# Kernel tuning notes

Hardware: AMD Instinct MI355X
Metric: run time of the kernel (lower is better)

## Reference

```python
import jax, jax.numpy as jnp
import numpy as np


def setup_inputs() -> dict:
    key = jax.random.key(0)
    ks = jax.random.split(key, 8)
    B, C, W, H = 4, 256, 64, 64
    Cq = C // 8
    return {
        "input": jax.random.normal(ks[0], (B, C, W, H), dtype=jnp.float32),
        "Wf": jax.random.normal(ks[1], (Cq, C), dtype=jnp.float32) * 0.05,
        "bf": jax.random.normal(ks[2], (Cq,), dtype=jnp.float32) * 0.05,
        "Wg": jax.random.normal(ks[3], (Cq, C), dtype=jnp.float32) * 0.05,
        "bg": jax.random.normal(ks[4], (Cq,), dtype=jnp.float32) * 0.05,
        "Wh": jax.random.normal(ks[5], (C, C), dtype=jnp.float32) * 0.05,
        "bh": jax.random.normal(ks[6], (C,), dtype=jnp.float32) * 0.05,
        "gamma": jax.random.normal(ks[7], (1,), dtype=jnp.float32),
    }


def reference(input, Wf, bf, Wg, bg, Wh, bh, gamma):
    # input: [B, C, W, H]; SAGAN self-attention over N = W*H spatial tokens.
    B, C, W, H = input.shape
    N = W * H
    x = input.reshape(B, C, N)
    # 1x1 Conv1d == per-token linear projection over channels.
    f = jnp.einsum('oc,bcn->bon', Wf, x) + bf[None, :, None]  # [B, C/8, N]
    g = jnp.einsum('oc,bcn->bon', Wg, x) + bg[None, :, None]  # [B, C/8, N]
    h = jnp.einsum('oc,bcn->bon', Wh, x) + bh[None, :, None]  # [B, C,   N]
    # s = f^T g -> [B, N, N]; softmax over last dim (columns / g-tokens).
    s = jnp.einsum('bon,bom->bnm', f, g)
    attention = jax.nn.softmax(s, axis=-1)
    # out = h @ attention^T : out[b,c,m] = sum_n h[b,c,n] * attention[b,m,n]
    out = jnp.einsum('bcn,bmn->bcm', h, attention)
    out = out.reshape(B, C, W, H)
    return gamma[0] * out + input
```

## Files before the change

### kernel.cpp

```cpp
#include <hip/hip_runtime.h>

typedef _Float16 half8 __attribute__((ext_vector_type(8)));
typedef _Float16 half4 __attribute__((ext_vector_type(4)));
typedef float floatx16 __attribute__((ext_vector_type(16)));

#define MFMA_F16(A, B, C) __builtin_amdgcn_mfma_f32_32x32x16_f16(A, B, C, 0, 0, 0)

constexpr int Bn = 4;
constexpr int Cc = 256;
constexpr int Cq = 32;
constexpr int Nn = 4096;
constexpr float LOG2E = 1.44269504088896340736f;


__device__ inline floatx16 zero16() {
  floatx16 z;
#pragma unroll
  for (int i = 0; i < 16; ++i) z[i] = 0.f;
  return z;
}

__global__ __launch_bounds__(256) void k_wconv(
    const float* __restrict__ Wf, const float* __restrict__ Wg,
    const float* __restrict__ Wh, _Float16* __restrict__ Wfh,
    _Float16* __restrict__ Wgh, _Float16* __restrict__ Whh) {
  int e = (blockIdx.x * 256 + threadIdx.x) * 4;
  const float* src;
  _Float16* dst;
  float sc = 1.f;
  if (e < 8192) { src = Wf + e; dst = Wfh + e; sc = LOG2E; }
  else if (e < 16384) { src = Wg + (e - 8192); dst = Wgh + (e - 8192); }
  else { src = Wh + (e - 16384); dst = Whh + (e - 16384); }
  float4 v = *(const float4*)src;
  half4 o;
  o[0] = (_Float16)(v.x * sc); o[1] = (_Float16)(v.y * sc);
  o[2] = (_Float16)(v.z * sc); o[3] = (_Float16)(v.w * sc);
  *(half4*)dst = o;
}

__global__ __launch_bounds__(256) void k_proj(
    const float* __restrict__ x,
    const _Float16* __restrict__ Wfh, const float* __restrict__ bf,
    const _Float16* __restrict__ Wgh, const float* __restrict__ bg,
    const _Float16* __restrict__ Whh, const float* __restrict__ bh,
    _Float16* __restrict__ Q, _Float16* __restrict__ K4,
    _Float16* __restrict__ V8) {
  int tid = threadIdx.x;
  int w = tid >> 6, lane = tid & 63;
  int ml = lane & 31, h = lane >> 5;
  int b = blockIdx.x >> 7, nt = blockIdx.x & 127;
  int n0 = nt * 32;
  const float* xb = x + (size_t)b * Cc * Nn + n0 + ml;

  for (int t = w; t < 10; t += 4) {
    const _Float16* W;
    const float* bias;
    float bscale = 1.f;
    int o0 = 0;
    if (t == 0) { W = Wfh; bias = bf; bscale = LOG2E; }
    else if (t == 1) { W = Wgh; bias = bg; }
    else { W = Whh + (size_t)(t - 2) * 32 * Cc; bias = bh + (t - 2) * 32; o0 = (t - 2) * 32; }

    floatx16 acc = zero16();
    const _Float16* wp = W + (size_t)ml * Cc + h * 8;
#pragma unroll
    for (int kc = 0; kc < 16; ++kc) {
      half8 a = *(const half8*)(wp + kc * 16);
      const float* xp = xb + (size_t)(kc * 16 + h * 8) * Nn;
      half8 bfr;
#pragma unroll
      for (int j = 0; j < 8; ++j) bfr[j] = (_Float16)xp[(size_t)j * Nn];
      acc = MFMA_F16(a, bfr, acc);
    }

    if (t == 0) {
      _Float16* op = Q + ((size_t)b * Nn + n0 + ml) * Cq;
#pragma unroll
      for (int qd = 0; qd < 4; ++qd) {
        float4 bq = *(const float4*)(bias + 8 * qd + 4 * h);
        const float* bqp = (const float*)&bq;
#pragma unroll
        for (int i = 0; i < 4; ++i) {
          int crow = i + 8 * qd + 4 * h;
          op[crow] = (_Float16)(acc[4 * qd + i] + bqp[i] * bscale);
        }
      }
    } else if (t == 1) {
#pragma unroll
      for (int qd = 0; qd < 4; ++qd) {
        float4 bq = *(const float4*)(bias + 8 * qd + 4 * h);
        const float* bqp = (const float*)&bq;
#pragma unroll
        for (int i = 0; i < 4; ++i) {
          int crow = i + 8 * qd + 4 * h;
          K4[(((size_t)b * 4 + (crow >> 3)) * Nn + n0 + ml) * 8 + (crow & 7)] =
              (_Float16)(acc[4 * qd + i] + bqp[i]);
        }
      }
    } else {
      size_t nb = (size_t)((n0 + ml) >> 3);
      _Float16* op = V8 + (((size_t)b * 512 + nb) * 256) * 8 + (ml & 7);
#pragma unroll
      for (int qd = 0; qd < 4; ++qd) {
        float4 bq = *(const float4*)(bias + 8 * qd + 4 * h);
        const float* bqp = (const float*)&bq;
#pragma unroll
        for (int i = 0; i < 4; ++i) {
          int crow = i + 8 * qd + 4 * h;
          op[(size_t)(o0 + crow) * 8] = (_Float16)(acc[4 * qd + i] + bqp[i]);
        }
      }
    }
  }
}

__global__ __launch_bounds__(512) void k_rowmax(const _Float16* __restrict__ Q,
                                                const _Float16* __restrict__ K4,
                                                float* __restrict__ M) {
  __shared__ float red[8][32];
  int tid = threadIdx.x, w = tid >> 6, lane = tid & 63;
  int ml = lane & 31, h = lane >> 5;
  int b = blockIdx.x >> 7, mt = blockIdx.x & 127;
  int m0 = mt * 32;
  const _Float16* qp = Q + ((size_t)b * Nn + m0 + ml) * Cq + h * 8;
  half8 qb0 = *(const half8*)(qp);
  half8 qb1 = *(const half8*)(qp + 16);
  const _Float16* kp0 = K4 + (((size_t)b * 4 + h) * Nn + w * 512 + ml) * 8;
  const _Float16* kp1 = K4 + (((size_t)b * 4 + 2 + h) * Nn + w * 512 + ml) * 8;
  float mx = -3.0e38f;
  for (int t = 0; t < 16; ++t) {
    floatx16 s = zero16();
    half8 k0 = *(const half8*)(kp0 + (size_t)t * 32 * 8);
    half8 k1 = *(const half8*)(kp1 + (size_t)t * 32 * 8);
    s = MFMA_F16(k0, qb0, s);
    s = MFMA_F16(k1, qb1, s);
#pragma unroll
    for (int i = 0; i < 16; ++i) mx = fmaxf(mx, s[i]);
  }
  mx = fmaxf(mx, __shfl_xor(mx, 32, 64));
  if (h == 0) red[w][ml] = mx;
  __syncthreads();
  if (tid < 32) {
    float m2 = red[0][tid];
#pragma unroll
    for (int i = 1; i < 8; ++i) m2 = fmaxf(m2, red[i][tid]);
    M[(size_t)b * Nn + m0 + tid] = m2;
  }
}

__global__ __launch_bounds__(512, 4) void k_attn(
    const _Float16* __restrict__ Q, const _Float16* __restrict__ K4,
    const _Float16* __restrict__ V8, const float* __restrict__ M,
    _Float16* __restrict__ Opart, float* __restrict__ lpart, int nspan) {
  __shared__ _Float16 P[2 * 64 * 128];
  __shared__ float lred[8][32];
  int tid = threadIdx.x, w = tid >> 6, lane = tid & 63;
  int ml = lane & 31, h = lane >> 5;
  int msub = w & 1, nq = w >> 1;
  int bx = blockIdx.x;
  int mt = bx & 63, b = (bx >> 6) & 3, nc = bx >> 8;
  int m0 = mt * 64;
  int nbase0 = nc * nspan;
  int sw = ml & 15;

  const _Float16* qp = Q + ((size_t)b * Nn + m0 + msub * 32 + ml) * Cq + h * 8;
  half8 qb0 = *(const half8*)(qp);
  half8 qb1 = *(const half8*)(qp + 16);
  float Mv = M[(size_t)b * Nn + m0 + msub * 32 + ml];
  float lacc = 0.f;

  const _Float16* k4b0 =
      K4 + (((size_t)b * 4 + h) * Nn + nbase0 + nq * 32 + ml) * 8;
  const _Float16* k4b1 =
      K4 + (((size_t)b * 4 + 2 + h) * Nn + nbase0 + nq * 32 + ml) * 8;

  int c0 = w * 32;
  const _Float16* v8b =
      V8 + (((size_t)b * 512 + (nbase0 >> 3)) * 256 + c0 + ml) * 8;

  floatx16 o0 = zero16(), o1 = zero16();
  int iters = nspan >> 7;
  _Float16* pwbase = &P[(msub * 32 + ml) * 128];
  const _Float16* pr0 = &P[ml * 128];
  const _Float16* pr1 = &P[(32 + ml) * 128];

  for (int it = 0; it < iters; ++it) {
    int bufo = (it & 1) * (64 * 128);
    {
      floatx16 s = zero16();
      half8 k0 = *(const half8*)(k4b0 + (size_t)it * 128 * 8);
      half8 k1 = *(const half8*)(k4b1 + (size_t)it * 128 * 8);
      s = MFMA_F16(k0, qb0, s);
      s = MFMA_F16(k1, qb1, s);
      _Float16* pw = pwbase + bufo;
#pragma unroll
      for (int q = 0; q < 4; ++q) {
        float p0 = exp2f(s[4 * q + 0] - Mv);
        float p1 = exp2f(s[4 * q + 1] - Mv);
        float p2 = exp2f(s[4 * q + 2] - Mv);
        float p3 = exp2f(s[4 * q + 3] - Mv);
        lacc += (p0 + p1) + (p2 + p3);
        half4 pk;
        pk[0] = (_Float16)p0; pk[1] = (_Float16)p1;
        pk[2] = (_Float16)p2; pk[3] = (_Float16)p3;
        *(half4*)(pw + ((nq * 4 + q) ^ sw) * 8 + 4 * h) = pk;
      }
    }
    __syncthreads();
    {
      const _Float16* vp = v8b + (size_t)it * 16 * 2048;
      const _Float16* p0b = pr0 + bufo;
      const _Float16* p1b = pr1 + bufo;
#pragma unroll
      for (int kc = 0; kc < 8; ++kc) {
        half8 vf = *(const half8*)(vp + (size_t)(kc * 2 + h) * 2048);
        int chunk = (kc * 2 + h) ^ sw;
        half8 pb0 = *(const half8*)(p0b + chunk * 8);
        half8 pb1 = *(const half8*)(p1b + chunk * 8);
        o0 = MFMA_F16(vf, pb0, o0);
        o1 = MFMA_F16(vf, pb1, o1);
      }
    }
  }

  lacc += __shfl_xor(lacc, 32, 64);
  if (h == 0) lred[w][ml] = lacc;
  __syncthreads();
  if (w < 2 && h == 0) {
    float lsum = lred[w][ml] + lred[w + 2][ml] + lred[w + 4][ml] + lred[w + 6][ml];
    lpart[((size_t)nc * Bn + b) * Nn + m0 + w * 32 + ml] = lsum;
  }

  _Float16* op0 = Opart + ((size_t)((size_t)nc * Bn + b) * Cc) * Nn + (m0 + ml);
#pragma unroll
  for (int r = 0; r < 16; ++r) {
    int c = c0 + (r & 3) + 8 * (r >> 2) + 4 * h;
    op0[(size_t)c * Nn] = (_Float16)o0[r];
    op0[(size_t)c * Nn + 32] = (_Float16)o1[r];
  }
}

__global__ __launch_bounds__(256) void k_fin(const _Float16* __restrict__ Op,
                                             const float* __restrict__ lp,
                                             const float* __restrict__ inp,
                                             const float* __restrict__ gamma,
                                             float* __restrict__ out, int NC) {
  int i4 = (blockIdx.x * 256 + threadIdx.x) * 4;
  int m = i4 & (Nn - 1);
  int bc = i4 >> 12;
  int b = bc >> 8;
  float ax = 0.f, ay = 0.f, az = 0.f, aw = 0.f;
  float lx = 0.f, ly = 0.f, lz = 0.f, lw = 0.f;
  for (int nc = 0; nc < NC; ++nc) {
    half4 o = *(const half4*)(Op + ((size_t)nc * Bn * Cc + bc) * Nn + m);
    float4 lv = *(const float4*)(lp + ((size_t)nc * Bn + b) * Nn + m);
    ax += (float)o[0]; ay += (float)o[1]; az += (float)o[2]; aw += (float)o[3];
    lx += lv.x; ly += lv.y; lz += lv.z; lw += lv.w;
  }
  float g = gamma[0];
  float4 xi = *(const float4*)(inp + (size_t)i4);
  float4 r;
  r.x = g * ax / lx + xi.x;
  r.y = g * ay / ly + xi.y;
  r.z = g * az / lz + xi.z;
  r.w = g * aw / lw + xi.w;
  *(float4*)(out + (size_t)i4) = r;
}

extern "C" void kernel_launch(void* const* d_in, const int* in_sizes, int n_in,
                              void* d_out, int out_size, void* d_ws,
                              size_t ws_size, hipStream_t stream) {
  const float* x = (const float*)d_in[0];
  const float* Wf = (const float*)d_in[1];
  const float* bf = (const float*)d_in[2];
  const float* Wg = (const float*)d_in[3];
  const float* bg = (const float*)d_in[4];
  const float* Wh = (const float*)d_in[5];
  const float* bh = (const float*)d_in[6];
  const float* gamma = (const float*)d_in[7];
  float* out = (float*)d_out;

  char* ws = (char*)d_ws;
  _Float16* Q  = (_Float16*)(ws);
  _Float16* K4 = (_Float16*)(ws + 1048576);
  _Float16* V8 = (_Float16*)(ws + 2097152);
  float*    M  = (float*)   (ws + 10485760);
  _Float16* Wfh = (_Float16*)(ws + 10551296);
  _Float16* Wgh = (_Float16*)(ws + 10567680);
  _Float16* Whh = (_Float16*)(ws + 10584064);
  float*    lpart = (float*)(ws + 10715136);
  _Float16* Opart = (_Float16*)(ws + 10846208);

  size_t base = 10846208u;
  int NC = (ws_size >= base + 2u * 8388608u) ? 2 : 1;
  int nspan = Nn / NC;

  k_wconv<<<dim3(80), dim3(256), 0, stream>>>(Wf, Wg, Wh, Wfh, Wgh, Whh);
  k_proj<<<dim3(512), dim3(256), 0, stream>>>(x, Wfh, bf, Wgh, bg, Whh, bh, Q, K4, V8);
  k_rowmax<<<dim3(512), dim3(512), 0, stream>>>(Q, K4, M);
  k_attn<<<dim3(NC * 256), dim3(512), 0, stream>>>(Q, K4, V8, M, Opart, lpart, nspan);
  k_fin<<<dim3(4096), dim3(256), 0, stream>>>(Opart, lpart, x, gamma, out, NC);
}
```

Baseline: 169.6 us.

## Stage x through LDS in projection, raise attn occupancy, split N into four chunks

The projection kernel now loads each 32-token x tile into shared memory with coalesced float4 reads and converts it to half fragments once. Previously every wave performed strided scalar global loads per MFMA. The attention kernel asks for 8 blocks per CU in its launch bounds, uses the hardware exp2 intrinsic, and packs to fp16 with round-toward-zero. The host picks up to 4 key chunks when the workspace allows, for more parallelism at the cost of extra partial buffers and more finalize work. The higher occupancy target may force register spills.

```diff
diff --git a/kernel.cpp b/kernel.cpp
--- a/kernel.cpp
+++ b/kernel.cpp
@@ -2,6 +2,8 @@
 
 typedef _Float16 half8 __attribute__((ext_vector_type(8)));
 typedef _Float16 half4 __attribute__((ext_vector_type(4)));
+typedef __fp16 f16x2 __attribute__((ext_vector_type(2)));
+typedef __fp16 f16x4 __attribute__((ext_vector_type(4)));
 typedef float floatx16 __attribute__((ext_vector_type(16)));
 
 #define MFMA_F16(A, B, C) __builtin_amdgcn_mfma_f32_32x32x16_f16(A, B, C, 0, 0, 0)
@@ -45,12 +47,38 @@
     const _Float16* __restrict__ Whh, const float* __restrict__ bh,
     _Float16* __restrict__ Q, _Float16* __restrict__ K4,
     _Float16* __restrict__ V8) {
+  __shared__ float xs[32][260];
   int tid = threadIdx.x;
   int w = tid >> 6, lane = tid & 63;
   int ml = lane & 31, h = lane >> 5;
   int b = blockIdx.x >> 7, nt = blockIdx.x & 127;
   int n0 = nt * 32;
-  const float* xb = x + (size_t)b * Cc * Nn + n0 + ml;
+
+  {
+    int c = tid >> 3;
+    int nl = (tid & 7) * 4;
+    const float* xp = x + (size_t)b * Cc * Nn + n0 + nl;
+#pragma unroll
+    for (int pass = 0; pass < 8; ++pass) {
+      int cc = c + pass * 32;
+      float4 v = *(const float4*)(xp + (size_t)cc * Nn);
+      xs[nl + 0][cc] = v.x;
+      xs[nl + 1][cc] = v.y;
+      xs[nl + 2][cc] = v.z;
+      xs[nl + 3][cc] = v.w;
+    }
+  }
+  __syncthreads();
+
+  half8 bfr[16];
+#pragma unroll
+  for (int kc = 0; kc < 16; ++kc) {
+    const float* xp = &xs[ml][kc * 16 + h * 8];
+    half8 f;
+#pragma unroll
+    for (int j = 0; j < 8; ++j) f[j] = (_Float16)xp[j];
+    bfr[kc] = f;
+  }
 
   for (int t = w; t < 10; t += 4) {
     const _Float16* W;
@@ -66,11 +94,7 @@
 #pragma unroll
     for (int kc = 0; kc < 16; ++kc) {
       half8 a = *(const half8*)(wp + kc * 16);
-      const float* xp = xb + (size_t)(kc * 16 + h * 8) * Nn;
-      half8 bfr;
-#pragma unroll
-      for (int j = 0; j < 8; ++j) bfr[j] = (_Float16)xp[(size_t)j * Nn];
-      acc = MFMA_F16(a, bfr, acc);
+      acc = MFMA_F16(a, bfr[kc], acc);
     }
 
     if (t == 0) {
@@ -148,7 +172,7 @@
   }
 }
 
-__global__ __launch_bounds__(512, 4) void k_attn(
+__global__ __launch_bounds__(512, 8) void k_attn(
     const _Float16* __restrict__ Q, const _Float16* __restrict__ K4,
     const _Float16* __restrict__ V8, const float* __restrict__ M,
     _Float16* __restrict__ Opart, float* __restrict__ lpart, int nspan) {
@@ -195,14 +219,15 @@
       _Float16* pw = pwbase + bufo;
 #pragma unroll
       for (int q = 0; q < 4; ++q) {
-        float p0 = exp2f(s[4 * q + 0] - Mv);
-        float p1 = exp2f(s[4 * q + 1] - Mv);
-        float p2 = exp2f(s[4 * q + 2] - Mv);
-        float p3 = exp2f(s[4 * q + 3] - Mv);
+        float p0 = __builtin_amdgcn_exp2f(s[4 * q + 0] - Mv);
+        float p1 = __builtin_amdgcn_exp2f(s[4 * q + 1] - Mv);
+        float p2 = __builtin_amdgcn_exp2f(s[4 * q + 2] - Mv);
+        float p3 = __builtin_amdgcn_exp2f(s[4 * q + 3] - Mv);
         lacc += (p0 + p1) + (p2 + p3);
-        half4 pk;
-        pk[0] = (_Float16)p0; pk[1] = (_Float16)p1;
-        pk[2] = (_Float16)p2; pk[3] = (_Float16)p3;
+        f16x4 pkv = __builtin_shufflevector(__builtin_amdgcn_cvt_pkrtz(p0, p1),
+                                            __builtin_amdgcn_cvt_pkrtz(p2, p3),
+                                            0, 1, 2, 3);
+        half4 pk = __builtin_bit_cast(half4, pkv);
         *(half4*)(pw + ((nq * 4 + q) ^ sw) * 8 + 4 * h) = pk;
       }
     }
@@ -288,12 +313,16 @@
   _Float16* Wfh = (_Float16*)(ws + 10551296);
   _Float16* Wgh = (_Float16*)(ws + 10567680);
   _Float16* Whh = (_Float16*)(ws + 10584064);
-  float*    lpart = (float*)(ws + 10715136);
-  _Float16* Opart = (_Float16*)(ws + 10846208);
-
-  size_t base = 10846208u;
-  int NC = (ws_size >= base + 2u * 8388608u) ? 2 : 1;
+
+  size_t base = 10715136u;
+  size_t per_chunk = 65536u + 8388608u;
+  int NC = 1;
+  if (ws_size >= base + 4u * per_chunk) NC = 4;
+  else if (ws_size >= base + 2u * per_chunk) NC = 2;
   int nspan = Nn / NC;
+
+  float*    lpart = (float*)(ws + base);
+  _Float16* Opart = (_Float16*)(ws + base + (size_t)NC * 65536u);
 
   k_wconv<<<dim3(80), dim3(256), 0, stream>>>(Wf, Wg, Wh, Wfh, Wgh, Whh);
   k_proj<<<dim3(512), dim3(256), 0, stream>>>(x, Wfh, bf, Wgh, bg, Whh, bh, Q, K4, V8);
```

After: 219.7 us. 1.3x slower.
